# Kernel tuning notes

Measured on AMD Instinct MI355X. Metric: run time of the kernel, lower is better.

## Reference

```python
import jax, jax.numpy as jnp
import numpy as np

NUM_NODES = 40000
NUM_EDGES = 400000
DIM = 128
NUM_REL = 502  # num_relation * 2
NUM_HEAD = 1


def setup_inputs() -> dict:
    key = jax.random.key(0)
    ks = jax.random.split(key, 16)
    d = DIM
    return {
        "curr_stat": jax.random.normal(ks[0], (NUM_NODES, d), jnp.float32),
        "last_stat": jax.random.normal(ks[1], (NUM_NODES, d), jnp.float32),
        "relemb_weight": jax.random.normal(ks[2], (NUM_REL, d), jnp.float32),
        "selfrel_weight": jax.random.normal(ks[3], (1, d), jnp.float32),
        "Wq": jax.random.normal(ks[4], (2 * d, d), jnp.float32) * (1.0 / np.sqrt(2 * d)),
        "bq": jax.random.normal(ks[5], (d,), jnp.float32) * 0.02,
        "Wk": jax.random.normal(ks[6], (2 * d, d), jnp.float32) * (1.0 / np.sqrt(2 * d)),
        "bk": jax.random.normal(ks[7], (d,), jnp.float32) * 0.02,
        "Wv": jax.random.normal(ks[8], (d, d), jnp.float32) * (1.0 / np.sqrt(d)),
        "bv": jax.random.normal(ks[9], (d,), jnp.float32) * 0.02,
        "dyn_weight": jax.random.normal(ks[10], (d, d), jnp.float32) * (1.0 / np.sqrt(d)),
        "edge_index": jax.random.randint(ks[11], (2, NUM_EDGES), 0, NUM_NODES, jnp.int32),
        "edge_type": jax.random.randint(ks[12], (NUM_EDGES,), 0, NUM_REL, jnp.int32),
    }


def _segment_softmax(scores, seg, num_segments):
    # scores: [E, H]; softmax over edges sharing the same destination segment
    m = jax.ops.segment_max(scores, seg, num_segments=num_segments)  # [N, H]
    e = jnp.exp(scores - m[seg])
    s = jax.ops.segment_sum(e, seg, num_segments=num_segments)  # [N, H]
    return e / s[seg]


def reference(curr_stat, last_stat, relemb_weight, selfrel_weight,
              Wq, bq, Wk, bk, Wv, bv, dyn_weight,
              edge_index, edge_type):
    N, D = curr_stat.shape
    H = NUM_HEAD
    HD = D // H

    # append self-loop edges for every node, with the dedicated self-relation
    loop = jnp.arange(N, dtype=edge_index.dtype)
    src = jnp.concatenate([edge_index[0], loop])  # [E_total]
    dst = jnp.concatenate([edge_index[1], loop])  # [E_total]
    type_emb = jnp.concatenate(
        [relemb_weight[edge_type], jnp.broadcast_to(selfrel_weight, (N, D))], axis=0)

    E = src.shape[0]
    # linear projections (x @ W + b); torch Linear stores W transposed, same math
    q = (jnp.concatenate([curr_stat[dst], type_emb], -1) @ Wq + bq).reshape(E, H, HD)
    k = (jnp.concatenate([last_stat[src], type_emb], -1) @ Wk + bk).reshape(E, H, HD)
    v = (last_stat[src] @ Wv + bv).reshape(E, H, HD)

    attn = jnp.sum(q * k, axis=-1) / np.sqrt(HD).astype(np.float32)  # [E, H]

    dyn_prob = _segment_softmax(attn, dst, N)   # [E, H]
    sta_prob = _segment_softmax(-attn, dst, N)  # [E, H]

    counts = jax.ops.segment_sum(jnp.ones((E,), jnp.float32), dst, num_segments=N)
    denom = jnp.maximum(counts, 1.0)[:, None]  # scatter-mean denominator

    feat_dyn = jax.ops.segment_sum((dyn_prob[..., None] * v).reshape(E, D), dst,
                                   num_segments=N) / denom
    feat_sta = jax.ops.segment_sum((sta_prob[..., None] * v).reshape(E, D), dst,
                                   num_segments=N) / denom

    # stack (feat_sta, feat_dyn @ dyn_weight) -> [2, N, D]
    return jnp.stack([feat_sta, feat_dyn @ dyn_weight])
```

## Files before the change

kernel.cpp:

```cpp
#include <hip/hip_runtime.h>
#include <hip/hip_bf16.h>
#include <math.h>

#define DIMC 128

typedef __attribute__((ext_vector_type(8))) short short8;
typedef __attribute__((ext_vector_type(4))) float floatx4;

static __device__ __forceinline__ unsigned pk2(float lo, float hi) {
    __hip_bfloat162 h = __float22bfloat162_rn(make_float2(lo, hi));
    return *(unsigned*)&h;
}
static __device__ __forceinline__ unsigned short f2bf(float x) {
    union { float f; unsigned int u; } v; v.f = x;
    unsigned int r = v.u + 0x7FFFu + ((v.u >> 16) & 1u);
    return (unsigned short)(r >> 16);
}
static __device__ __forceinline__ float2 bf2f2(unsigned int u) {
    union { unsigned int i; float f; } a, b;
    a.i = u << 16; b.i = u & 0xFFFF0000u;
    return make_float2(a.f, b.f);
}

struct PrepArgs {
    const float* W[6];
    unsigned short* F[6];
    const float* relemb; const float* selfrel;
    float* TypeEmb;
    int* deg;
    int R; int N;
};

__global__ __launch_bounds__(64) void prep_all(PrepArgs a)
{
    int b = blockIdx.x;
    int lane = threadIdx.x;
    if (b < 192) {
        int mat = b >> 5, ts = b & 31;
        int s = ts & 3, t = ts >> 2;
        int q = lane >> 4, c = lane & 15;
        const float* W = a.W[mat];
        unsigned short o[8];
        #pragma unroll
        for (int j = 0; j < 8; ++j)
            o[j] = f2bf(W[(long)(s * 32 + q * 8 + j) * DIMC + t * 16 + c]);
        uint4 u;
        u.x = (unsigned)o[0] | ((unsigned)o[1] << 16);
        u.y = (unsigned)o[2] | ((unsigned)o[3] << 16);
        u.z = (unsigned)o[4] | ((unsigned)o[5] << 16);
        u.w = (unsigned)o[6] | ((unsigned)o[7] << 16);
        ((uint4*)a.F[mat])[ts * 64 + lane] = u;
    } else if (b < 192 + a.R + 1) {
        int r = b - 192;
        const float* src = (r < a.R) ? (a.relemb + (long)r * DIMC) : a.selfrel;
        float2 v = ((const float2*)src)[lane];
        ((float2*)(a.TypeEmb + (long)r * DIMC))[lane] = v;
    } else {
        int i = (b - (192 + a.R + 1)) * 64 + lane;
        if (i < a.N) a.deg[i] = 0;
    }
}

struct GemmM5 {
    const float*          Af[5];
    const unsigned short* Ab[5];
    const unsigned short* F[5];
    const float*          bias[5];
    float*                outf[5];
    unsigned short*       outb[5];
    int                   ostride[5];
    int                   ooff[5];
    int                   M[5];
};

__global__ __launch_bounds__(256) void gemm_mfma(GemmM5 g)
{
    const int which = blockIdx.y;
    const int M = g.M[which];
    if (blockIdx.x * 64 >= M) return;

    const float*          __restrict__ Af   = g.Af[which];
    const unsigned short* __restrict__ Ab   = g.Ab[which];
    const unsigned short* __restrict__ F    = g.F[which];
    const float*          __restrict__ bias = g.bias[which];
    float*          __restrict__ outf = g.outf[which];
    unsigned short* __restrict__ outb = g.outb[which];
    const int ostride = g.ostride[which];
    const int ooff    = g.ooff[which];

    const int wave = threadIdx.x >> 6;
    const int lane = threadIdx.x & 63;
    const int q = lane >> 4, c = lane & 15;
    const int rowbase = blockIdx.x * 64 + wave * 16;

    short8 wf[8][4];
    const uint4* Fp = (const uint4*)F;
    #pragma unroll
    for (int t = 0; t < 8; ++t)
        #pragma unroll
        for (int s = 0; s < 4; ++s) {
            uint4 u = Fp[(t * 4 + s) * 64 + lane];
            wf[t][s] = *(short8*)&u;
        }

    floatx4 acc[8];
    #pragma unroll
    for (int t = 0; t < 8; ++t) {
        float b = bias ? bias[t * 16 + c] : 0.0f;
        acc[t] = (floatx4){b, b, b, b};
    }

    int rowA = rowbase + c; if (rowA > M - 1) rowA = M - 1;
    short8 af[4];
    if (Af) {
        const float* Ar = Af + (long)rowA * DIMC + q * 8;
        #pragma unroll
        for (int s = 0; s < 4; ++s) {
            float4 x0 = *(const float4*)(Ar + s * 32);
            float4 x1 = *(const float4*)(Ar + s * 32 + 4);
            uint4 u;
            u.x = pk2(x0.x, x0.y);
            u.y = pk2(x0.z, x0.w);
            u.z = pk2(x1.x, x1.y);
            u.w = pk2(x1.z, x1.w);
            af[s] = *(short8*)&u;
        }
    } else {
        const unsigned short* Ar = Ab + (long)rowA * DIMC + q * 8;
        #pragma unroll
        for (int s = 0; s < 4; ++s) {
            uint4 u = *(const uint4*)(Ar + s * 32);
            af[s] = *(short8*)&u;
        }
    }

    #pragma unroll
    for (int t = 0; t < 8; ++t)
        #pragma unroll
        for (int s = 0; s < 4; ++s)
            acc[t] = __builtin_amdgcn_mfma_f32_16x16x32_bf16(af[s], wf[t][s], acc[t], 0, 0, 0);

    if (outf) {
        #pragma unroll
        for (int t = 0; t < 8; ++t)
            #pragma unroll
            for (int r = 0; r < 4; ++r) {
                int row = rowbase + q * 4 + r;
                if (row < M)
                    outf[(long)row * DIMC + t * 16 + c] = acc[t][r];
            }
    } else {
        #pragma unroll
        for (int t = 0; t < 8; ++t)
            #pragma unroll
            for (int r = 0; r < 4; ++r) {
                float other = __shfl_xor(acc[t][r], 1);
                int row = rowbase + q * 4 + r;
                if ((lane & 1) == 0 && row < M) {
                    unsigned word = pk2(acc[t][r], other);
                    ((unsigned*)outb)[((long)row * 64 + t * 8 + (c >> 1))
                                      * (long)ostride + ooff] = word;
                }
            }
    }
}

__global__ void hist_kernel(const int* __restrict__ dst, int* __restrict__ deg, int E) {
    int e = blockIdx.x * blockDim.x + threadIdx.x;
    if (e < E) atomicAdd(&deg[dst[e]], 1);
}

__global__ __launch_bounds__(256) void partial_sums(const int* __restrict__ deg,
                                                    int* __restrict__ partial, int N)
{
    __shared__ int sh[256];
    int t = threadIdx.x;
    int beg = blockIdx.x * 1024 + t * 4;
    int s = 0;
    if (beg + 3 < N) { int4 v = *(const int4*)(deg + beg); s = v.x + v.y + v.z + v.w; }
    else { for (int j = 0; j < 4; ++j) if (beg + j < N) s += deg[beg + j]; }
    sh[t] = s;
    __syncthreads();
    for (int d = 128; d >= 1; d >>= 1) {
        if (t < d) sh[t] += sh[t + d];
        __syncthreads();
    }
    if (t == 0) partial[blockIdx.x] = sh[0];
}

__global__ __launch_bounds__(256) void scan_partials(int* __restrict__ partial, int nb)
{
    __shared__ int sh[256];
    int t = threadIdx.x;
    sh[t] = (t < nb) ? partial[t] : 0;
    __syncthreads();
    for (int d = 1; d < 256; d <<= 1) {
        int v = (t >= d) ? sh[t - d] : 0;
        __syncthreads();
        sh[t] += v;
        __syncthreads();
    }
    if (t < nb) partial[t] = (t == 0) ? 0 : sh[t - 1];
}

__global__ __launch_bounds__(256) void write_offsets(const int* __restrict__ deg,
                                                     const int* __restrict__ partial,
                                                     int* __restrict__ offs,
                                                     int* __restrict__ cursor, int N)
{
    __shared__ int sh[256];
    int t = threadIdx.x;
    int beg = blockIdx.x * 1024 + t * 4;
    int d0 = 0, d1 = 0, d2 = 0, d3 = 0;
    if (beg + 3 < N) { int4 v = *(const int4*)(deg + beg); d0 = v.x; d1 = v.y; d2 = v.z; d3 = v.w; }
    else {
        if (beg < N)     d0 = deg[beg];
        if (beg + 1 < N) d1 = deg[beg + 1];
        if (beg + 2 < N) d2 = deg[beg + 2];
        if (beg + 3 < N) d3 = deg[beg + 3];
    }
    int s = d0 + d1 + d2 + d3;
    sh[t] = s;
    __syncthreads();
    for (int d = 1; d < 256; d <<= 1) {
        int v = (t >= d) ? sh[t - d] : 0;
        __syncthreads();
        sh[t] += v;
        __syncthreads();
    }
    int base = partial[blockIdx.x] + sh[t] - s;
    int o0 = base, o1 = o0 + d0, o2 = o1 + d1, o3 = o2 + d2;
    if (beg < N)     { offs[beg]     = o0; cursor[beg]     = o0; }
    if (beg + 1 < N) { offs[beg + 1] = o1; cursor[beg + 1] = o1; }
    if (beg + 2 < N) { offs[beg + 2] = o2; cursor[beg + 2] = o2; }
    if (beg + 3 < N) { offs[beg + 3] = o3; cursor[beg + 3] = o3; }
}

__global__ void scatter_kernel(const int* __restrict__ src, const int* __restrict__ dst,
                               const int* __restrict__ etype, int* __restrict__ cursor,
                               int2* __restrict__ sedge, int E)
{
    int e = blockIdx.x * blockDim.x + threadIdx.x;
    if (e < E) {
        int d = dst[e];
        int p = atomicAdd(&cursor[d], 1);
        sedge[p] = make_int2(src[e], etype[e]);
    }
}

__global__ __launch_bounds__(256) void node_kernel(
    const float* __restrict__ Qn,
    const uint4* __restrict__ KV4,
    const uint4* __restrict__ QK4,
    const int* __restrict__ offs, const int* __restrict__ deg,
    const int2* __restrict__ sedge,
    float* __restrict__ out_sta, uint2* __restrict__ feat_dyn,
    int N, int R)
{
    int n = (blockIdx.x * blockDim.x + threadIdx.x) >> 6;
    int lane = threadIdx.x & 63;
    if (n >= N) return;
    const int hl = lane & 31;
    const int h  = lane >> 5;

    const float cs = 0.08838834764831845f * 1.4426950408889634f;
    int base = offs[n];
    int dcnt = deg[n];

    float4 qn = ((const float4*)(Qn + (long)n * DIMC))[hl];

    uint4 kvs = KV4[(unsigned)n * 32u + hl];
    uint4 qks = QK4[(unsigned)R * 32u + hl];
    {
        float2 k0 = bf2f2(kvs.x), k1 = bf2f2(kvs.z);
        float2 qr0 = bf2f2(qks.x), qr1 = bf2f2(qks.z);
        float2 kr0 = bf2f2(qks.y), kr1 = bf2f2(qks.w);
        float p = (qn.x + qr0.x) * (k0.x + kr0.x)
                + (qn.y + qr0.y) * (k0.y + kr0.y)
                + (qn.z + qr1.x) * (k1.x + kr1.x)
                + (qn.w + qr1.y) * (k1.y + kr1.y);
        #pragma unroll
        for (int m = 16; m >= 1; m >>= 1) p += __shfl_xor(p, m);
        kvs.x = __float_as_uint(p);
        qks.x = 0;
        float a_self = p * cs;
        float2 v0 = bf2f2(kvs.y), v1 = bf2f2(kvs.w);
        float m_d, s_d, m_s, s_s; float4 accd, accs;
        if (h == 0) {
            m_d = a_self;  s_d = 1.0f;
            m_s = -a_self; s_s = 1.0f;
            accd = make_float4(v0.x, v0.y, v1.x, v1.y);
            accs = accd;
        } else {
            m_d = -1e30f; s_d = 0.0f;
            m_s = -1e30f; s_s = 0.0f;
            accd = make_float4(0.f, 0.f, 0.f, 0.f);
            accs = accd;
        }

        int T = (dcnt + 3) >> 2;
        for (int it = 0; it < T; ++it) {
            int iA = 4 * it + 2 * h, iB = iA + 1;
            bool vA = iA < dcnt, vB = iB < dcnt;
            int2 eA = sedge[vA ? (base + iA) : 0];
            int2 eB = sedge[vB ? (base + iB) : 0];
            uint4 kvA = KV4[(unsigned)eA.x * 32u + hl];
            uint4 kvB = KV4[(unsigned)eB.x * 32u + hl];
            uint4 qkA = QK4[(unsigned)eA.y * 32u + hl];
            uint4 qkB = QK4[(unsigned)eB.y * 32u + hl];

            float2 ka0 = bf2f2(kvA.x), ka1 = bf2f2(kvA.z);
            float2 qa0 = bf2f2(qkA.x), qa1 = bf2f2(qkA.z);
            float2 ra0 = bf2f2(qkA.y), ra1 = bf2f2(qkA.w);
            float pA = (qn.x + qa0.x) * (ka0.x + ra0.x)
                     + (qn.y + qa0.y) * (ka0.y + ra0.y)
                     + (qn.z + qa1.x) * (ka1.x + ra1.x)
                     + (qn.w + qa1.y) * (ka1.y + ra1.y);
            float2 kb0 = bf2f2(kvB.x), kb1 = bf2f2(kvB.z);
            float2 qb0 = bf2f2(qkB.x), qb1 = bf2f2(qkB.z);
            float2 rb0 = bf2f2(qkB.y), rb1 = bf2f2(qkB.w);
            float pB = (qn.x + qb0.x) * (kb0.x + rb0.x)
                     + (qn.y + qb0.y) * (kb0.y + rb0.y)
                     + (qn.z + qb1.x) * (kb1.x + rb1.x)
                     + (qn.w + qb1.y) * (kb1.y + rb1.y);
            #pragma unroll
            for (int m = 16; m >= 1; m >>= 1) {
                pA += __shfl_xor(pA, m);
                pB += __shfl_xor(pB, m);
            }
            float aA = pA * cs, aB = pB * cs;
            float dA = vA ? aA : -1e30f, dB = vB ? aB : -1e30f;
            float nA = vA ? -aA : -1e30f, nB = vB ? -aB : -1e30f;

            float2 va0 = bf2f2(kvA.y), va1 = bf2f2(kvA.w);
            float2 vb0 = bf2f2(kvB.y), vb1 = bf2f2(kvB.w);

            {
                float mn = fmaxf(m_d, fmaxf(dA, dB));
                float f  = exp2f(m_d - mn);
                float wA = vA ? exp2f(dA - mn) : 0.0f;
                float wB = vB ? exp2f(dB - mn) : 0.0f;
                s_d = fmaf(s_d, f, wA + wB);
                accd.x = fmaf(accd.x, f, fmaf(wA, va0.x, wB * vb0.x));
                accd.y = fmaf(accd.y, f, fmaf(wA, va0.y, wB * vb0.y));
                accd.z = fmaf(accd.z, f, fmaf(wA, va1.x, wB * vb1.x));
                accd.w = fmaf(accd.w, f, fmaf(wA, va1.y, wB * vb1.y));
                m_d = mn;
            }
            {
                float mn = fmaxf(m_s, fmaxf(nA, nB));
                float f  = exp2f(m_s - mn);
                float wA = vA ? exp2f(nA - mn) : 0.0f;
                float wB = vB ? exp2f(nB - mn) : 0.0f;
                s_s = fmaf(s_s, f, wA + wB);
                accs.x = fmaf(accs.x, f, fmaf(wA, va0.x, wB * vb0.x));
                accs.y = fmaf(accs.y, f, fmaf(wA, va0.y, wB * vb0.y));
                accs.z = fmaf(accs.z, f, fmaf(wA, va1.x, wB * vb1.x));
                accs.w = fmaf(accs.w, f, fmaf(wA, va1.y, wB * vb1.y));
                m_s = mn;
            }
        }

        {
            float mo = __shfl_xor(m_d, 32), so = __shfl_xor(s_d, 32);
            float4 ao;
            ao.x = __shfl_xor(accd.x, 32); ao.y = __shfl_xor(accd.y, 32);
            ao.z = __shfl_xor(accd.z, 32); ao.w = __shfl_xor(accd.w, 32);
            float M = fmaxf(m_d, mo);
            float f0 = exp2f(m_d - M), f1 = exp2f(mo - M);
            s_d = fmaf(s_d, f0, so * f1);
            accd.x = fmaf(accd.x, f0, ao.x * f1);
            accd.y = fmaf(accd.y, f0, ao.y * f1);
            accd.z = fmaf(accd.z, f0, ao.z * f1);
            accd.w = fmaf(accd.w, f0, ao.w * f1);
        }
        {
            float mo = __shfl_xor(m_s, 32), so = __shfl_xor(s_s, 32);
            float4 ao;
            ao.x = __shfl_xor(accs.x, 32); ao.y = __shfl_xor(accs.y, 32);
            ao.z = __shfl_xor(accs.z, 32); ao.w = __shfl_xor(accs.w, 32);
            float M = fmaxf(m_s, mo);
            float f0 = exp2f(m_s - M), f1 = exp2f(mo - M);
            s_s = fmaf(s_s, f0, so * f1);
            accs.x = fmaf(accs.x, f0, ao.x * f1);
            accs.y = fmaf(accs.y, f0, ao.y * f1);
            accs.z = fmaf(accs.z, f0, ao.z * f1);
            accs.w = fmaf(accs.w, f0, ao.w * f1);
        }

        if (h == 0) {
            float denom = (float)(dcnt + 1);
            float id_ = 1.0f / (s_d * denom);
            float is_ = 1.0f / (s_s * denom);
            ((float4*)(out_sta + (long)n * DIMC))[hl] =
                make_float4(accs.x * is_, accs.y * is_, accs.z * is_, accs.w * is_);
            feat_dyn[(unsigned)n * 32u + hl] =
                make_uint2(pk2(accd.x * id_, accd.y * id_), pk2(accd.z * id_, accd.w * id_));
        }
    }
}

extern "C" void kernel_launch(void* const* d_in, const int* in_sizes, int n_in,
                              void* d_out, int out_size, void* d_ws, size_t ws_size,
                              hipStream_t stream)
{
    const float* curr    = (const float*)d_in[0];
    const float* last    = (const float*)d_in[1];
    const float* relemb  = (const float*)d_in[2];
    const float* selfrel = (const float*)d_in[3];
    const float* Wq      = (const float*)d_in[4];
    const float* bq      = (const float*)d_in[5];
    const float* Wk      = (const float*)d_in[6];
    const float* bk      = (const float*)d_in[7];
    const float* Wv      = (const float*)d_in[8];
    const float* bv      = (const float*)d_in[9];
    const float* dynw    = (const float*)d_in[10];
    const int*   eidx    = (const int*)d_in[11];
    const int*   etype   = (const int*)d_in[12];
    float* out = (float*)d_out;

    const int N = in_sizes[0] / DIMC;
    const int E = in_sizes[12];
    const int R = in_sizes[2] / DIMC;
    const int* esrc = eidx;
    const int* edst = eidx + E;

    char* wp = (char*)d_ws;
    auto alloc = [&](size_t bytes) { char* r = wp; wp += (bytes + 15) & ~(size_t)15; return r; };
    size_t nd = (size_t)N * DIMC;
    float*          Qn    = (float*)alloc(nd * 4);
    uint4*          KV    = (uint4*)alloc((size_t)N * 32 * 16);
    unsigned short* Fdb   = (unsigned short*)alloc(nd * 2);
    uint4*          QKre  = (uint4*)alloc((size_t)(R + 1) * 32 * 16);
    float*          TypeEmb = (float*)alloc((size_t)(R + 2) * DIMC * 4);
    unsigned short* FW[6];
    for (int m = 0; m < 6; ++m) FW[m] = (unsigned short*)alloc(2048 * 8 * 2);
    int*            deg   = (int*)alloc((size_t)N * 4);
    int*            offs  = (int*)alloc((size_t)N * 4);
    int*            cursor= (int*)alloc((size_t)N * 4);
    int2*           sedge = (int2*)alloc((size_t)E * 8);
    int*            partial = (int*)alloc(256 * 4);

    const int gblk = N / 64;
    const int sblk = (N + 1023) / 1024;

    PrepArgs pa;
    pa.W[0] = Wq;   pa.W[1] = Wk;   pa.W[2] = Wv;
    pa.W[3] = dynw; pa.W[4] = Wq + (size_t)DIMC * DIMC; pa.W[5] = Wk + (size_t)DIMC * DIMC;
    for (int m = 0; m < 6; ++m) pa.F[m] = FW[m];
    pa.relemb = relemb; pa.selfrel = selfrel; pa.TypeEmb = TypeEmb;
    pa.deg = deg; pa.R = R; pa.N = N;
    int pgrid = 192 + (R + 1) + (N + 63) / 64;
    hipLaunchKernelGGL(prep_all, dim3(pgrid), dim3(64), 0, stream, pa);

    hipLaunchKernelGGL(hist_kernel, dim3((E + 255) / 256), dim3(256), 0, stream, edst, deg, E);
    hipLaunchKernelGGL(partial_sums, dim3(sblk), dim3(256), 0, stream, deg, partial, N);
    hipLaunchKernelGGL(scan_partials, dim3(1), dim3(256), 0, stream, partial, sblk);
    hipLaunchKernelGGL(write_offsets, dim3(sblk), dim3(256), 0, stream,
                       deg, partial, offs, cursor, N);
    hipLaunchKernelGGL(scatter_kernel, dim3((E + 255) / 256), dim3(256), 0, stream,
                       esrc, edst, etype, cursor, sedge, E);

    GemmM5 g5;
    for (int s = 0; s < 5; ++s) { g5.Ab[s] = nullptr; g5.outf[s] = nullptr; g5.outb[s] = nullptr; }
    g5.Af[0] = curr;    g5.F[0] = FW[0]; g5.bias[0] = nullptr; g5.outf[0] = Qn;
    g5.ostride[0] = 1;  g5.ooff[0] = 0;  g5.M[0] = N;
    g5.Af[1] = last;    g5.F[1] = FW[1]; g5.bias[1] = nullptr; g5.outb[1] = (unsigned short*)KV;
    g5.ostride[1] = 2;  g5.ooff[1] = 0;  g5.M[1] = N;
    g5.Af[2] = last;    g5.F[2] = FW[2]; g5.bias[2] = bv;      g5.outb[2] = (unsigned short*)KV;
    g5.ostride[2] = 2;  g5.ooff[2] = 1;  g5.M[2] = N;
    g5.Af[3] = TypeEmb; g5.F[3] = FW[4]; g5.bias[3] = bq;      g5.outb[3] = (unsigned short*)QKre;
    g5.ostride[3] = 2;  g5.ooff[3] = 0;  g5.M[3] = R + 1;
    g5.Af[4] = TypeEmb; g5.F[4] = FW[5]; g5.bias[4] = bk;      g5.outb[4] = (unsigned short*)QKre;
    g5.ostride[4] = 2;  g5.ooff[4] = 1;  g5.M[4] = R + 1;
    hipLaunchKernelGGL(gemm_mfma, dim3(gblk, 5), dim3(256), 0, stream, g5);

    hipLaunchKernelGGL(node_kernel, dim3((N + 3) / 4), dim3(256), 0, stream,
                       Qn, KV, QKre, offs, deg, sedge, out, (uint2*)Fdb, N, R);

    GemmM5 gf;
    for (int s = 0; s < 5; ++s) { gf.Af[s] = nullptr; gf.Ab[s] = nullptr; gf.outf[s] = nullptr; gf.outb[s] = nullptr; gf.M[s] = 0; }
    gf.Ab[0] = Fdb; gf.F[0] = FW[3]; gf.bias[0] = nullptr; gf.outf[0] = out + nd;
    gf.ostride[0] = 1; gf.ooff[0] = 0; gf.M[0] = N;
    hipLaunchKernelGGL(gemm_mfma, dim3(gblk, 1), dim3(256), 0, stream, gf);
}
```

Before: 243.9 us.

## Fuse histogram into GEMM, merge scan kernels, simplify node softmax with DPP reductions

Moves the degree histogram into an extra grid row of the projection GEMM launch and merges the partial scan with offset writing, cutting kernel launches. Edge source and type indices are pre-shifted to byte offsets so gathers skip address multiplies. The node kernel drops running-max tracking in both segment softmaxes, uses packed float2 math and DPP-based 32-lane reductions. Removing max subtraction risks overflow or precision loss if attention scores are large.

```diff
diff --git a/kernel.cpp b/kernel.cpp
--- a/kernel.cpp
+++ b/kernel.cpp
@@ -6,6 +6,7 @@
 
 typedef __attribute__((ext_vector_type(8))) short short8;
 typedef __attribute__((ext_vector_type(4))) float floatx4;
+typedef __attribute__((ext_vector_type(2))) float f32x2;
 
 static __device__ __forceinline__ unsigned pk2(float lo, float hi) {
     __hip_bfloat162 h = __float22bfloat162_rn(make_float2(lo, hi));
@@ -16,10 +17,24 @@
     unsigned int r = v.u + 0x7FFFu + ((v.u >> 16) & 1u);
     return (unsigned short)(r >> 16);
 }
-static __device__ __forceinline__ float2 bf2f2(unsigned int u) {
+static __device__ __forceinline__ f32x2 bfp(unsigned int u) {
     union { unsigned int i; float f; } a, b;
     a.i = u << 16; b.i = u & 0xFFFF0000u;
-    return make_float2(a.f, b.f);
+    f32x2 r; r.x = a.f; r.y = b.f; return r;
+}
+
+template<int CTRL>
+static __device__ __forceinline__ float dpp_add(float x) {
+    int y = __builtin_amdgcn_update_dpp(0, __float_as_int(x), CTRL, 0xF, 0xF, true);
+    return x + __int_as_float(y);
+}
+static __device__ __forceinline__ float red32(float p) {
+    p = dpp_add<0xB1>(p);
+    p = dpp_add<0x4E>(p);
+    p = dpp_add<0x141>(p);
+    p = dpp_add<0x140>(p);
+    p += __shfl_xor(p, 16);
+    return p;
 }
 
 struct PrepArgs {
@@ -71,10 +86,20 @@
     int                   ostride[5];
     int                   ooff[5];
     int                   M[5];
+    const int*            hist_dst;
+    int*                  hist_deg;
+    int                   hist_E;
 };
 
 __global__ __launch_bounds__(256) void gemm_mfma(GemmM5 g)
 {
+    if (blockIdx.y == 5) {
+        int i = blockIdx.x * blockDim.x + threadIdx.x;
+        int stride = gridDim.x * blockDim.x;
+        for (; i < g.hist_E; i += stride) atomicAdd(&g.hist_deg[g.hist_dst[i]], 1);
+        return;
+    }
+
     const int which = blockIdx.y;
     const int M = g.M[which];
     if (blockIdx.x * 64 >= M) return;
@@ -165,11 +190,6 @@
     }
 }
 
-__global__ void hist_kernel(const int* __restrict__ dst, int* __restrict__ deg, int E) {
-    int e = blockIdx.x * blockDim.x + threadIdx.x;
-    if (e < E) atomicAdd(&deg[dst[e]], 1);
-}
-
 __global__ __launch_bounds__(256) void partial_sums(const int* __restrict__ deg,
                                                     int* __restrict__ partial, int N)
 {
@@ -188,28 +208,20 @@
     if (t == 0) partial[blockIdx.x] = sh[0];
 }
 
-__global__ __launch_bounds__(256) void scan_partials(int* __restrict__ partial, int nb)
+__global__ __launch_bounds__(256) void scan_write_offsets(const int* __restrict__ deg,
+                                                          const int* __restrict__ partial,
+                                                          int* __restrict__ offs,
+                                                          int* __restrict__ cursor, int N, int nb)
 {
     __shared__ int sh[256];
+    __shared__ int sbase;
     int t = threadIdx.x;
-    sh[t] = (t < nb) ? partial[t] : 0;
-    __syncthreads();
-    for (int d = 1; d < 256; d <<= 1) {
-        int v = (t >= d) ? sh[t - d] : 0;
-        __syncthreads();
-        sh[t] += v;
-        __syncthreads();
-    }
-    if (t < nb) partial[t] = (t == 0) ? 0 : sh[t - 1];
-}
-
-__global__ __launch_bounds__(256) void write_offsets(const int* __restrict__ deg,
-                                                     const int* __restrict__ partial,
-                                                     int* __restrict__ offs,
-                                                     int* __restrict__ cursor, int N)
-{
-    __shared__ int sh[256];
-    int t = threadIdx.x;
+    if (t < 64) {
+        int v = (t < nb && t < (int)blockIdx.x) ? partial[t] : 0;
+        #pragma unroll
+        for (int d = 32; d >= 1; d >>= 1) v += __shfl_xor(v, d);
+        if (t == 0) sbase = v;
+    }
     int beg = blockIdx.x * 1024 + t * 4;
     int d0 = 0, d1 = 0, d2 = 0, d3 = 0;
     if (beg + 3 < N) { int4 v = *(const int4*)(deg + beg); d0 = v.x; d1 = v.y; d2 = v.z; d3 = v.w; }
@@ -228,7 +240,7 @@
         sh[t] += v;
         __syncthreads();
     }
-    int base = partial[blockIdx.x] + sh[t] - s;
+    int base = sbase + sh[t] - s;
     int o0 = base, o1 = o0 + d0, o2 = o1 + d1, o3 = o2 + d2;
     if (beg < N)     { offs[beg]     = o0; cursor[beg]     = o0; }
     if (beg + 1 < N) { offs[beg + 1] = o1; cursor[beg + 1] = o1; }
@@ -244,14 +256,14 @@
     if (e < E) {
         int d = dst[e];
         int p = atomicAdd(&cursor[d], 1);
-        sedge[p] = make_int2(src[e], etype[e]);
+        sedge[p] = make_int2(src[e] << 9, etype[e] << 9);
     }
 }
 
 __global__ __launch_bounds__(256) void node_kernel(
     const float* __restrict__ Qn,
-    const uint4* __restrict__ KV4,
-    const uint4* __restrict__ QK4,
+    const char*  __restrict__ KVb,
+    const char*  __restrict__ QKb,
     const int* __restrict__ offs, const int* __restrict__ deg,
     const int2* __restrict__ sedge,
     float* __restrict__ out_sta, uint2* __restrict__ feat_dyn,
@@ -262,41 +274,34 @@
     if (n >= N) return;
     const int hl = lane & 31;
     const int h  = lane >> 5;
-
-    const float cs = 0.08838834764831845f * 1.4426950408889634f;
+    const int lo16 = hl << 4;
+
+    const float cs2 = 0.08838834764831845f * 1.4426950408889634f;
     int base = offs[n];
     int dcnt = deg[n];
 
-    float4 qn = ((const float4*)(Qn + (long)n * DIMC))[hl];
-
-    uint4 kvs = KV4[(unsigned)n * 32u + hl];
-    uint4 qks = QK4[(unsigned)R * 32u + hl];
+    float4 qn4 = ((const float4*)(Qn + (long)n * DIMC))[hl];
+    f32x2 q01; q01.x = qn4.x; q01.y = qn4.y;
+    f32x2 q23; q23.x = qn4.z; q23.y = qn4.w;
+
+    uint4 kvs = *(const uint4*)(KVb + ((long)n << 9) + lo16);
+    uint4 qks = *(const uint4*)(QKb + ((long)R << 9) + lo16);
     {
-        float2 k0 = bf2f2(kvs.x), k1 = bf2f2(kvs.z);
-        float2 qr0 = bf2f2(qks.x), qr1 = bf2f2(qks.z);
-        float2 kr0 = bf2f2(qks.y), kr1 = bf2f2(qks.w);
-        float p = (qn.x + qr0.x) * (k0.x + kr0.x)
-                + (qn.y + qr0.y) * (k0.y + kr0.y)
-                + (qn.z + qr1.x) * (k1.x + kr1.x)
-                + (qn.w + qr1.y) * (k1.y + kr1.y);
-        #pragma unroll
-        for (int m = 16; m >= 1; m >>= 1) p += __shfl_xor(p, m);
-        kvs.x = __float_as_uint(p);
-        qks.x = 0;
-        float a_self = p * cs;
-        float2 v0 = bf2f2(kvs.y), v1 = bf2f2(kvs.w);
-        float m_d, s_d, m_s, s_s; float4 accd, accs;
-        if (h == 0) {
-            m_d = a_self;  s_d = 1.0f;
-            m_s = -a_self; s_s = 1.0f;
-            accd = make_float4(v0.x, v0.y, v1.x, v1.y);
-            accs = accd;
-        } else {
-            m_d = -1e30f; s_d = 0.0f;
-            m_s = -1e30f; s_s = 0.0f;
-            accd = make_float4(0.f, 0.f, 0.f, 0.f);
-            accs = accd;
-        }
+        f32x2 s0 = q01 + bfp(qks.x);
+        f32x2 s1 = q23 + bfp(qks.z);
+        f32x2 k0 = bfp(kvs.x) + bfp(qks.y);
+        f32x2 k1 = bfp(kvs.z) + bfp(qks.w);
+        f32x2 dp = s0 * k0;
+        dp += s1 * k1;
+        float p = red32(dp.x + dp.y);
+        float t = p * cs2;
+        float wd = (h == 0) ? exp2f(t)  : 0.0f;
+        float ws = (h == 0) ? exp2f(-t) : 0.0f;
+        f32x2 v0 = bfp(kvs.y), v1 = bfp(kvs.w);
+
+        float s_d = wd, s_s = ws;
+        f32x2 accd0 = v0 * wd, accd1 = v1 * wd;
+        f32x2 accs0 = v0 * ws, accs1 = v1 * ws;
 
         int T = (dcnt + 3) >> 2;
         for (int it = 0; it < T; ++it) {
@@ -304,98 +309,58 @@
             bool vA = iA < dcnt, vB = iB < dcnt;
             int2 eA = sedge[vA ? (base + iA) : 0];
             int2 eB = sedge[vB ? (base + iB) : 0];
-            uint4 kvA = KV4[(unsigned)eA.x * 32u + hl];
-            uint4 kvB = KV4[(unsigned)eB.x * 32u + hl];
-            uint4 qkA = QK4[(unsigned)eA.y * 32u + hl];
-            uint4 qkB = QK4[(unsigned)eB.y * 32u + hl];
-
-            float2 ka0 = bf2f2(kvA.x), ka1 = bf2f2(kvA.z);
-            float2 qa0 = bf2f2(qkA.x), qa1 = bf2f2(qkA.z);
-            float2 ra0 = bf2f2(qkA.y), ra1 = bf2f2(qkA.w);
-            float pA = (qn.x + qa0.x) * (ka0.x + ra0.x)
-                     + (qn.y + qa0.y) * (ka0.y + ra0.y)
-                     + (qn.z + qa1.x) * (ka1.x + ra1.x)
-                     + (qn.w + qa1.y) * (ka1.y + ra1.y);
-            float2 kb0 = bf2f2(kvB.x), kb1 = bf2f2(kvB.z);
-            float2 qb0 = bf2f2(qkB.x), qb1 = bf2f2(qkB.z);
-            float2 rb0 = bf2f2(qkB.y), rb1 = bf2f2(qkB.w);
-            float pB = (qn.x + qb0.x) * (kb0.x + rb0.x)
-                     + (qn.y + qb0.y) * (kb0.y + rb0.y)
-                     + (qn.z + qb1.x) * (kb1.x + rb1.x)
-                     + (qn.w + qb1.y) * (kb1.y + rb1.y);
-            #pragma unroll
-            for (int m = 16; m >= 1; m >>= 1) {
-                pA += __shfl_xor(pA, m);
-                pB += __shfl_xor(pB, m);
-            }
-            float aA = pA * cs, aB = pB * cs;
-            float dA = vA ? aA : -1e30f, dB = vB ? aB : -1e30f;
-            float nA = vA ? -aA : -1e30f, nB = vB ? -aB : -1e30f;
-
-            float2 va0 = bf2f2(kvA.y), va1 = bf2f2(kvA.w);
-            float2 vb0 = bf2f2(kvB.y), vb1 = bf2f2(kvB.w);
-
-            {
-                float mn = fmaxf(m_d, fmaxf(dA, dB));
-                float f  = exp2f(m_d - mn);
-                float wA = vA ? exp2f(dA - mn) : 0.0f;
-                float wB = vB ? exp2f(dB - mn) : 0.0f;
-                s_d = fmaf(s_d, f, wA + wB);
-                accd.x = fmaf(accd.x, f, fmaf(wA, va0.x, wB * vb0.x));
-                accd.y = fmaf(accd.y, f, fmaf(wA, va0.y, wB * vb0.y));
-                accd.z = fmaf(accd.z, f, fmaf(wA, va1.x, wB * vb1.x));
-                accd.w = fmaf(accd.w, f, fmaf(wA, va1.y, wB * vb1.y));
-                m_d = mn;
-            }
-            {
-                float mn = fmaxf(m_s, fmaxf(nA, nB));
-                float f  = exp2f(m_s - mn);
-                float wA = vA ? exp2f(nA - mn) : 0.0f;
-                float wB = vB ? exp2f(nB - mn) : 0.0f;
-                s_s = fmaf(s_s, f, wA + wB);
-                accs.x = fmaf(accs.x, f, fmaf(wA, va0.x, wB * vb0.x));
-                accs.y = fmaf(accs.y, f, fmaf(wA, va0.y, wB * vb0.y));
-                accs.z = fmaf(accs.z, f, fmaf(wA, va1.x, wB * vb1.x));
-                accs.w = fmaf(accs.w, f, fmaf(wA, va1.y, wB * vb1.y));
-                m_s = mn;
-            }
+            uint4 kvA = *(const uint4*)(KVb + eA.x + lo16);
+            uint4 qkA = *(const uint4*)(QKb + eA.y + lo16);
+            uint4 kvB = *(const uint4*)(KVb + eB.x + lo16);
+            uint4 qkB = *(const uint4*)(QKb + eB.y + lo16);
+
+            f32x2 a0 = q01 + bfp(qkA.x), a1 = q23 + bfp(qkA.z);
+            f32x2 ka0 = bfp(kvA.x) + bfp(qkA.y), ka1 = bfp(kvA.z) + bfp(qkA.w);
+            f32x2 da = a0 * ka0;
+            da += a1 * ka1;
+            float pA = da.x + da.y;
+
+            f32x2 b0 = q01 + bfp(qkB.x), b1 = q23 + bfp(qkB.z);
+            f32x2 kb0 = bfp(kvB.x) + bfp(qkB.y), kb1 = bfp(kvB.z) + bfp(qkB.w);
+            f32x2 db = b0 * kb0;
+            db += b1 * kb1;
+            float pB = db.x + db.y;
+
+            pA = red32(pA);
+            pB = red32(pB);
+            float tA = pA * cs2, tB = pB * cs2;
+
+            float wdA = vA ? exp2f(tA)  : 0.0f;
+            float wsA = vA ? exp2f(-tA) : 0.0f;
+            float wdB = vB ? exp2f(tB)  : 0.0f;
+            float wsB = vB ? exp2f(-tB) : 0.0f;
+
+            s_d += wdA + wdB;
+            s_s += wsA + wsB;
+
+            f32x2 va0 = bfp(kvA.y), va1 = bfp(kvA.w);
+            f32x2 vb0 = bfp(kvB.y), vb1 = bfp(kvB.w);
+            accd0 += va0 * wdA;  accd0 += vb0 * wdB;
+            accd1 += va1 * wdA;  accd1 += vb1 * wdB;
+            accs0 += va0 * wsA;  accs0 += vb0 * wsB;
+            accs1 += va1 * wsA;  accs1 += vb1 * wsB;
         }
 
-        {
-            float mo = __shfl_xor(m_d, 32), so = __shfl_xor(s_d, 32);
-            float4 ao;
-            ao.x = __shfl_xor(accd.x, 32); ao.y = __shfl_xor(accd.y, 32);
-            ao.z = __shfl_xor(accd.z, 32); ao.w = __shfl_xor(accd.w, 32);
-            float M = fmaxf(m_d, mo);
-            float f0 = exp2f(m_d - M), f1 = exp2f(mo - M);
-            s_d = fmaf(s_d, f0, so * f1);
-            accd.x = fmaf(accd.x, f0, ao.x * f1);
-            accd.y = fmaf(accd.y, f0, ao.y * f1);
-            accd.z = fmaf(accd.z, f0, ao.z * f1);
-            accd.w = fmaf(accd.w, f0, ao.w * f1);
-        }
-        {
-            float mo = __shfl_xor(m_s, 32), so = __shfl_xor(s_s, 32);
-            float4 ao;
-            ao.x = __shfl_xor(accs.x, 32); ao.y = __shfl_xor(accs.y, 32);
-            ao.z = __shfl_xor(accs.z, 32); ao.w = __shfl_xor(accs.w, 32);
-            float M = fmaxf(m_s, mo);
-            float f0 = exp2f(m_s - M), f1 = exp2f(mo - M);
-            s_s = fmaf(s_s, f0, so * f1);
-            accs.x = fmaf(accs.x, f0, ao.x * f1);
-            accs.y = fmaf(accs.y, f0, ao.y * f1);
-            accs.z = fmaf(accs.z, f0, ao.z * f1);
-            accs.w = fmaf(accs.w, f0, ao.w * f1);
-        }
+        s_d += __shfl_xor(s_d, 32);
+        s_s += __shfl_xor(s_s, 32);
+        accd0.x += __shfl_xor(accd0.x, 32); accd0.y += __shfl_xor(accd0.y, 32);
+        accd1.x += __shfl_xor(accd1.x, 32); accd1.y += __shfl_xor(accd1.y, 32);
+        accs0.x += __shfl_xor(accs0.x, 32); accs0.y += __shfl_xor(accs0.y, 32);
+        accs1.x += __shfl_xor(accs1.x, 32); accs1.y += __shfl_xor(accs1.y, 32);
 
         if (h == 0) {
             float denom = (float)(dcnt + 1);
             float id_ = 1.0f / (s_d * denom);
             float is_ = 1.0f / (s_s * denom);
             ((float4*)(out_sta + (long)n * DIMC))[hl] =
-                make_float4(accs.x * is_, accs.y * is_, accs.z * is_, accs.w * is_);
+                make_float4(accs0.x * is_, accs0.y * is_, accs1.x * is_, accs1.y * is_);
             feat_dyn[(unsigned)n * 32u + hl] =
-                make_uint2(pk2(accd.x * id_, accd.y * id_), pk2(accd.z * id_, accd.w * id_));
+                make_uint2(pk2(accd0.x * id_, accd0.y * id_), pk2(accd1.x * id_, accd1.y * id_));
         }
     }
 }
@@ -453,14 +418,6 @@
     int pgrid = 192 + (R + 1) + (N + 63) / 64;
     hipLaunchKernelGGL(prep_all, dim3(pgrid), dim3(64), 0, stream, pa);
 
-    hipLaunchKernelGGL(hist_kernel, dim3((E + 255) / 256), dim3(256), 0, stream, edst, deg, E);
-    hipLaunchKernelGGL(partial_sums, dim3(sblk), dim3(256), 0, stream, deg, partial, N);
-    hipLaunchKernelGGL(scan_partials, dim3(1), dim3(256), 0, stream, partial, sblk);
-    hipLaunchKernelGGL(write_offsets, dim3(sblk), dim3(256), 0, stream,
-                       deg, partial, offs, cursor, N);
-    hipLaunchKernelGGL(scatter_kernel, dim3((E + 255) / 256), dim3(256), 0, stream,
-                       esrc, edst, etype, cursor, sedge, E);
-
     GemmM5 g5;
     for (int s = 0; s < 5; ++s) { g5.Ab[s] = nullptr; g5.outf[s] = nullptr; g5.outb[s] = nullptr; }
     g5.Af[0] = curr;    g5.F[0] = FW[0]; g5.bias[0] = nullptr; g5.outf[0] = Qn;
@@ -473,14 +430,23 @@
     g5.ostride[3] = 2;  g5.ooff[3] = 0;  g5.M[3] = R + 1;
     g5.Af[4] = TypeEmb; g5.F[4] = FW[5]; g5.bias[4] = bk;      g5.outb[4] = (unsigned short*)QKre;
     g5.ostride[4] = 2;  g5.ooff[4] = 1;  g5.M[4] = R + 1;
-    hipLaunchKernelGGL(gemm_mfma, dim3(gblk, 5), dim3(256), 0, stream, g5);
+    g5.hist_dst = edst; g5.hist_deg = deg; g5.hist_E = E;
+    hipLaunchKernelGGL(gemm_mfma, dim3(gblk, 6), dim3(256), 0, stream, g5);
+
+    hipLaunchKernelGGL(partial_sums, dim3(sblk), dim3(256), 0, stream, deg, partial, N);
+    hipLaunchKernelGGL(scan_write_offsets, dim3(sblk), dim3(256), 0, stream,
+                       deg, partial, offs, cursor, N, sblk);
+    hipLaunchKernelGGL(scatter_kernel, dim3((E + 255) / 256), dim3(256), 0, stream,
+                       esrc, edst, etype, cursor, sedge, E);
 
     hipLaunchKernelGGL(node_kernel, dim3((N + 3) / 4), dim3(256), 0, stream,
-                       Qn, KV, QKre, offs, deg, sedge, out, (uint2*)Fdb, N, R);
+                       Qn, (const char*)KV, (const char*)QKre, offs, deg, sedge,
+                       out, (uint2*)Fdb, N, R);
 
     GemmM5 gf;
     for (int s = 0; s < 5; ++s) { gf.Af[s] = nullptr; gf.Ab[s] = nullptr; gf.outf[s] = nullptr; gf.outb[s] = nullptr; gf.M[s] = 0; }
     gf.Ab[0] = Fdb; gf.F[0] = FW[3]; gf.bias[0] = nullptr; gf.outf[0] = out + nd;
     gf.ostride[0] = 1; gf.ooff[0] = 0; gf.M[0] = N;
+    gf.hist_dst = edst; gf.hist_deg = deg; gf.hist_E = 0;
     hipLaunchKernelGGL(gemm_mfma, dim3(gblk, 1), dim3(256), 0, stream, gf);
 }
```

Result: faster. 225.4 us (-7.6%).
